# Optimization experiments

Measured on AMD Instinct MI355X. Metric: run time of the kernel, lower is better.

Reference implementation:

```python
import jax, jax.numpy as jnp
import numpy as np

B, N, D_MEM, D_HID = 64, 65536, 1024, 1024


def setup_inputs() -> dict:
    key = jax.random.key(0)
    k1, k2, k3 = jax.random.split(key, 3)
    memory_bank = jax.random.normal(k1, (N, D_MEM), dtype=jnp.float32)
    decoder_state = jax.random.normal(k2, (B, D_HID), dtype=jnp.float32)
    # nn.Linear(memory_bank_size -> hidden_size, bias=False): weight [D_HID, D_MEM]
    W = jax.random.normal(k3, (D_HID, D_MEM), dtype=jnp.float32) / np.sqrt(D_MEM)
    # ragged tree sizes summing exactly to N (concrete, built on host)
    rng = np.random.default_rng(0)
    lens = rng.integers(512, 1536, size=B).astype(np.float64)
    lens = np.maximum(1, np.floor(lens * N / lens.sum()).astype(np.int64))
    lens[-1] += N - lens.sum()
    return {
        "memory_bank": memory_bank,
        "decoder_state": decoder_state,
        "W": W,
        "tree_node_num_lst": jnp.asarray(lens, dtype=jnp.int64),
    }


def reference(memory_bank, decoder_state, W, tree_node_num_lst):
    # segment id per node: tree index it belongs to (total_repeat_length keeps it jit-able)
    n_total = memory_bank.shape[0]
    batch = decoder_state.shape[0]
    seg = jnp.repeat(jnp.arange(batch), tree_node_num_lst, total_repeat_length=n_total)  # [N]
    # memory_project: one big GEMM instead of per-tree launches
    enc = memory_bank @ W.T                                  # [N, D_HID]
    # per-node score = <decoder_state[tree], enc[node]>
    scores = jnp.sum(enc * decoder_state[seg], axis=-1)      # [N]
    # segment (per-tree) stable softmax
    m = jax.ops.segment_max(scores, seg, num_segments=batch)  # [B]
    e = jnp.exp(scores - m[seg])                              # [N]
    z = jax.ops.segment_sum(e, seg, num_segments=batch)       # [B]
    attn = e / z[seg]                                         # [N]
    # context = attn-weighted sum of raw memory bank per tree
    context = jax.ops.segment_sum(attn[:, None] * memory_bank, seg, num_segments=batch)  # [B, D_MEM]
    return context
```

## Files before the change

### kernel.cpp

```cpp
#include <hip/hip_runtime.h>
#include <math.h>

#define B_TREES 64
#define N_NODES 65536
#define D 1024
#define D4 (D/4)

#define CHUNK 64
#define SUB 8
#define NSUB (CHUNK/SUB)
#define NCHUNK (N_NODES/CHUNK)
#define NSLOT (2*NCHUNK)

__global__ void offsets_kernel(const int* __restrict__ lens32, int* __restrict__ off) {
    if (threadIdx.x == 0 && blockIdx.x == 0) {
        long long s32 = 0;
        for (int b = 0; b < B_TREES; ++b) s32 += lens32[b];
        const bool is32 = (s32 == (long long)N_NODES);
        int acc = 0;
        off[0] = 0;
        for (int b = 0; b < B_TREES; ++b) {
            int len = is32 ? lens32[b] : (int)(((const long long*)lens32)[b]);
            acc += len;
            off[b + 1] = acc;
        }
    }
}

__global__ void v_kernel(const float* __restrict__ ds, const float* __restrict__ W,
                         float* __restrict__ v) {
    const int m  = blockIdx.x * 256 + threadIdx.x;
    const int b0 = blockIdx.y * 4;
    const int h0 = blockIdx.z * 128;
    float acc[4] = {0.f, 0.f, 0.f, 0.f};
    for (int h = h0; h < h0 + 128; ++h) {
        float wv = W[h * D + m];
        #pragma unroll
        for (int j = 0; j < 4; ++j)
            acc[j] += ds[(b0 + j) * D + h] * wv;
    }
    #pragma unroll
    for (int j = 0; j < 4; ++j)
        atomicAdd(&v[(b0 + j) * D + m], acc[j]);
}

__global__ __launch_bounds__(256) void fused_kernel(
    const float4* __restrict__ mb, const float4* __restrict__ v,
    const int* __restrict__ off,
    float* __restrict__ m_arr, float* __restrict__ z_arr,
    int* __restrict__ seg_arr, float4* __restrict__ vec)
{
    __shared__ float4 smb[SUB * D4];
    __shared__ float  ssc[SUB];
    __shared__ int    sinfo[2];

    const int tid  = threadIdx.x;
    const int wave = tid >> 6;
    const int lane = tid & 63;
    const int c    = blockIdx.x;
    const int n0   = c * CHUNK;

    if (tid == 0) {
        int lo = 0, hi = B_TREES - 1;
        while (lo < hi) { int mid = (lo + hi + 1) >> 1; if (off[mid] <= n0) lo = mid; else hi = mid - 1; }
        sinfo[0] = lo;
        const int nxt = off[lo + 1];
        sinfo[1] = (nxt < n0 + CHUNK) ? nxt : 0x7fffffff;
    }
    __syncthreads();
    const int sa   = sinfo[0];
    const int cutg = sinfo[1];
    const bool two = (cutg != 0x7fffffff);

    float  m0 = -INFINITY, z0 = 0.f, m1 = -INFINITY, z1 = 0.f;
    float4 a0 = make_float4(0.f, 0.f, 0.f, 0.f);
    float4 a1 = make_float4(0.f, 0.f, 0.f, 0.f);

    float4 vr0, vr1, vr2, vr3;
    int vcur = -1;

    for (int st = 0; st < NSUB; ++st) {
        const int nb = n0 + st * SUB;
        #pragma unroll
        for (int k = 0; k < SUB; ++k)
            smb[k * D4 + tid] = mb[(size_t)(nb + k) * D4 + tid];
        __syncthreads();

        #pragma unroll
        for (int q = 0; q < 2; ++q) {
            const int k  = wave * 2 + q;
            const int sg = (nb + k < cutg) ? sa : sa + 1;
            if (sg != vcur) {
                vcur = sg;
                vr0 = v[(size_t)sg * D4 +   0 + lane];
                vr1 = v[(size_t)sg * D4 +  64 + lane];
                vr2 = v[(size_t)sg * D4 + 128 + lane];
                vr3 = v[(size_t)sg * D4 + 192 + lane];
            }
            const float4 b0v = smb[k * D4 +   0 + lane];
            const float4 b1v = smb[k * D4 +  64 + lane];
            const float4 b2v = smb[k * D4 + 128 + lane];
            const float4 b3v = smb[k * D4 + 192 + lane];
            float acc = b0v.x*vr0.x + b0v.y*vr0.y + b0v.z*vr0.z + b0v.w*vr0.w;
            acc      += b1v.x*vr1.x + b1v.y*vr1.y + b1v.z*vr1.z + b1v.w*vr1.w;
            acc      += b2v.x*vr2.x + b2v.y*vr2.y + b2v.z*vr2.z + b2v.w*vr2.w;
            acc      += b3v.x*vr3.x + b3v.y*vr3.y + b3v.z*vr3.z + b3v.w*vr3.w;
            #pragma unroll
            for (int o = 32; o > 0; o >>= 1) acc += __shfl_down(acc, o, 64);
            if (lane == 0) ssc[k] = acc;
        }
        __syncthreads();

        #pragma unroll
        for (int k = 0; k < SUB; ++k) {
            const float  s    = ssc[k];
            const float4 arow = smb[k * D4 + tid];
            if (nb + k < cutg) {
                if (s > m0) {
                    const float sc = __expf(m0 - s);
                    z0 *= sc; a0.x *= sc; a0.y *= sc; a0.z *= sc; a0.w *= sc;
                    m0 = s;
                }
                const float w = __expf(s - m0);
                z0 += w;
                a0.x += w * arow.x; a0.y += w * arow.y; a0.z += w * arow.z; a0.w += w * arow.w;
            } else {
                if (s > m1) {
                    const float sc = __expf(m1 - s);
                    z1 *= sc; a1.x *= sc; a1.y *= sc; a1.z *= sc; a1.w *= sc;
                    m1 = s;
                }
                const float w = __expf(s - m1);
                z1 += w;
                a1.x += w * arow.x; a1.y += w * arow.y; a1.z += w * arow.z; a1.w += w * arow.w;
            }
        }
        __syncthreads();
    }

    const int slot0 = 2 * c, slot1 = 2 * c + 1;
    vec[(size_t)slot0 * D4 + tid] = a0;
    if (tid == 0) { m_arr[slot0] = m0; z_arr[slot0] = z0; seg_arr[slot0] = sa; }
    if (two) {
        vec[(size_t)slot1 * D4 + tid] = a1;
        if (tid == 0) { m_arr[slot1] = m1; z_arr[slot1] = z1; seg_arr[slot1] = sa + 1; }
    } else if (tid == 0) {
        seg_arr[slot1] = -1;
    }
}

__global__ __launch_bounds__(256) void combine_kernel(
    const int* __restrict__ off, const float* __restrict__ m_arr,
    const float* __restrict__ z_arr, const int* __restrict__ seg_arr,
    const float4* __restrict__ vec, float4* __restrict__ out)
{
    const int b = blockIdx.x, t = threadIdx.x;
    const int s0 = off[b], s1 = off[b + 1];
    const int c0 = s0 / CHUNK, c1 = (s1 - 1) / CHUNK;

    float mseg = -INFINITY;
    for (int cc = c0; cc <= c1; ++cc) {
        #pragma unroll
        for (int j = 0; j < 2; ++j) {
            const int sl = 2 * cc + j;
            if (seg_arr[sl] == b) mseg = fmaxf(mseg, m_arr[sl]);
        }
    }
    float zseg = 0.f;
    float4 acc = make_float4(0.f, 0.f, 0.f, 0.f);
    for (int cc = c0; cc <= c1; ++cc) {
        #pragma unroll
        for (int j = 0; j < 2; ++j) {
            const int sl = 2 * cc + j;
            if (seg_arr[sl] == b) {
                const float sc = __expf(m_arr[sl] - mseg);
                zseg += sc * z_arr[sl];
                const float4 vv = vec[(size_t)sl * D4 + t];
                acc.x += sc * vv.x; acc.y += sc * vv.y;
                acc.z += sc * vv.z; acc.w += sc * vv.w;
            }
        }
    }
    const float inv = 1.f / zseg;
    acc.x *= inv; acc.y *= inv; acc.z *= inv; acc.w *= inv;
    out[(size_t)b * D4 + t] = acc;
}

extern "C" void kernel_launch(void* const* d_in, const int* in_sizes, int n_in,
                              void* d_out, int out_size, void* d_ws, size_t ws_size,
                              hipStream_t stream) {
    const float* mb   = (const float*)d_in[0];
    const float* ds   = (const float*)d_in[1];
    const float* W    = (const float*)d_in[2];
    const int*   lens = (const int*)d_in[3];
    float*       out  = (float*)d_out;

    char*  ws      = (char*)d_ws;
    int*   off     = (int*)ws;
    float* v       = (float*)(ws + 512);
    float* m_arr   = (float*)(ws + 512 + 64 * D * 4);
    float* z_arr   = m_arr + NSLOT;
    int*   seg_arr = (int*)(z_arr + NSLOT);
    float* vec     = (float*)((char*)(seg_arr + NSLOT));

    hipMemsetAsync(v, 0, 64 * D * sizeof(float), stream);

    offsets_kernel<<<1, 64, 0, stream>>>(lens, off);

    {
        dim3 grid(4, 16, 8);
        v_kernel<<<grid, 256, 0, stream>>>(ds, W, v);
    }

    fused_kernel<<<NCHUNK, 256, 0, stream>>>(
        (const float4*)mb, (const float4*)v, off, m_arr, z_arr, seg_arr, (float4*)vec);

    combine_kernel<<<B_TREES, 256, 0, stream>>>(
        off, m_arr, z_arr, seg_arr, (const float4*)vec, (float4*)out);
}
```

Measured before the change: 406.3 us.

## Prefetch memory bank rows into registers, drop memset and offsets kernel

```diff
diff --git a/kernel.cpp b/kernel.cpp
--- a/kernel.cpp
+++ b/kernel.cpp
@@ -11,27 +11,36 @@
 #define NSUB (CHUNK/SUB)
 #define NCHUNK (N_NODES/CHUNK)
 #define NSLOT (2*NCHUNK)
-
-__global__ void offsets_kernel(const int* __restrict__ lens32, int* __restrict__ off) {
-    if (threadIdx.x == 0 && blockIdx.x == 0) {
-        long long s32 = 0;
-        for (int b = 0; b < B_TREES; ++b) s32 += lens32[b];
-        const bool is32 = (s32 == (long long)N_NODES);
-        int acc = 0;
-        off[0] = 0;
-        for (int b = 0; b < B_TREES; ++b) {
-            int len = is32 ? lens32[b] : (int)(((const long long*)lens32)[b]);
-            acc += len;
-            off[b + 1] = acc;
-        }
-    }
-}
-
-__global__ void v_kernel(const float* __restrict__ ds, const float* __restrict__ W,
-                         float* __restrict__ v) {
+#define VZ 8
+
+__device__ __forceinline__ void block_offsets(const int* __restrict__ lens32,
+                                              int* __restrict__ soff,
+                                              int tid, int lane) {
+    if ((tid >> 6) == 0) {
+        long long x32 = (long long)lens32[lane];
+        long long tot = x32;
+        #pragma unroll
+        for (int o = 32; o > 0; o >>= 1) tot += __shfl_xor(tot, o, 64);
+        int len = (tot == (long long)N_NODES) ? (int)x32
+                                              : (int)(((const long long*)lens32)[lane]);
+        int scan = len;
+        #pragma unroll
+        for (int o = 1; o < 64; o <<= 1) {
+            int y = __shfl_up(scan, o, 64);
+            if (lane >= o) scan += y;
+        }
+        soff[lane + 1] = scan;
+        if (lane == 0) soff[0] = 0;
+    }
+}
+
+__global__ __launch_bounds__(256) void v_kernel(const float* __restrict__ ds,
+                                                const float* __restrict__ W,
+                                                float* __restrict__ v_part) {
     const int m  = blockIdx.x * 256 + threadIdx.x;
     const int b0 = blockIdx.y * 4;
-    const int h0 = blockIdx.z * 128;
+    const int z  = blockIdx.z;
+    const int h0 = z * 128;
     float acc[4] = {0.f, 0.f, 0.f, 0.f};
     for (int h = h0; h < h0 + 128; ++h) {
         float wv = W[h * D + m];
@@ -41,18 +50,18 @@
     }
     #pragma unroll
     for (int j = 0; j < 4; ++j)
-        atomicAdd(&v[(b0 + j) * D + m], acc[j]);
-}
-
-__global__ __launch_bounds__(256) void fused_kernel(
-    const float4* __restrict__ mb, const float4* __restrict__ v,
-    const int* __restrict__ off,
+        v_part[((size_t)(z * B_TREES + b0 + j)) * D + m] = acc[j];
+}
+
+__global__ __launch_bounds__(256, 4) void fused_kernel(
+    const float4* __restrict__ mb, const float4* __restrict__ v_part,
+    const int* __restrict__ lens32,
     float* __restrict__ m_arr, float* __restrict__ z_arr,
     int* __restrict__ seg_arr, float4* __restrict__ vec)
 {
     __shared__ float4 smb[SUB * D4];
     __shared__ float  ssc[SUB];
-    __shared__ int    sinfo[2];
+    __shared__ int    soff[B_TREES + 1];
 
     const int tid  = threadIdx.x;
     const int wave = tid >> 6;
@@ -60,16 +69,19 @@
     const int c    = blockIdx.x;
     const int n0   = c * CHUNK;
 
-    if (tid == 0) {
-        int lo = 0, hi = B_TREES - 1;
-        while (lo < hi) { int mid = (lo + hi + 1) >> 1; if (off[mid] <= n0) lo = mid; else hi = mid - 1; }
-        sinfo[0] = lo;
-        const int nxt = off[lo + 1];
-        sinfo[1] = (nxt < n0 + CHUNK) ? nxt : 0x7fffffff;
-    }
+    float4 pf[SUB];
+    #pragma unroll
+    for (int k = 0; k < SUB; ++k)
+        pf[k] = mb[(size_t)(n0 + k) * D4 + tid];
+
+    block_offsets(lens32, soff, tid, lane);
     __syncthreads();
-    const int sa   = sinfo[0];
-    const int cutg = sinfo[1];
+
+    int lo = 0, hi = B_TREES - 1;
+    while (lo < hi) { int mid = (lo + hi + 1) >> 1; if (soff[mid] <= n0) lo = mid; else hi = mid - 1; }
+    const int sa   = lo;
+    const int nxt  = soff[sa + 1];
+    const int cutg = (nxt < n0 + CHUNK) ? nxt : 0x7fffffff;
     const bool two = (cutg != 0x7fffffff);
 
     float  m0 = -INFINITY, z0 = 0.f, m1 = -INFINITY, z1 = 0.f;
@@ -81,10 +93,18 @@
 
     for (int st = 0; st < NSUB; ++st) {
         const int nb = n0 + st * SUB;
+
         #pragma unroll
         for (int k = 0; k < SUB; ++k)
-            smb[k * D4 + tid] = mb[(size_t)(nb + k) * D4 + tid];
+            smb[k * D4 + tid] = pf[k];
         __syncthreads();
+
+        if (st + 1 < NSUB) {
+            const int nb2 = nb + SUB;
+            #pragma unroll
+            for (int k = 0; k < SUB; ++k)
+                pf[k] = mb[(size_t)(nb2 + k) * D4 + tid];
+        }
 
         #pragma unroll
         for (int q = 0; q < 2; ++q) {
@@ -92,10 +112,16 @@
             const int sg = (nb + k < cutg) ? sa : sa + 1;
             if (sg != vcur) {
                 vcur = sg;
-                vr0 = v[(size_t)sg * D4 +   0 + lane];
-                vr1 = v[(size_t)sg * D4 +  64 + lane];
-                vr2 = v[(size_t)sg * D4 + 128 + lane];
-                vr3 = v[(size_t)sg * D4 + 192 + lane];
+                vr0 = make_float4(0.f,0.f,0.f,0.f); vr1 = vr0; vr2 = vr0; vr3 = vr0;
+                #pragma unroll
+                for (int z = 0; z < VZ; ++z) {
+                    const float4* vp = v_part + (size_t)(z * B_TREES + sg) * D4;
+                    float4 t;
+                    t = vp[  0 + lane]; vr0.x+=t.x; vr0.y+=t.y; vr0.z+=t.z; vr0.w+=t.w;
+                    t = vp[ 64 + lane]; vr1.x+=t.x; vr1.y+=t.y; vr1.z+=t.z; vr1.w+=t.w;
+                    t = vp[128 + lane]; vr2.x+=t.x; vr2.y+=t.y; vr2.z+=t.z; vr2.w+=t.w;
+                    t = vp[192 + lane]; vr3.x+=t.x; vr3.y+=t.y; vr3.z+=t.z; vr3.w+=t.w;
+                }
             }
             const float4 b0v = smb[k * D4 +   0 + lane];
             const float4 b1v = smb[k * D4 +  64 + lane];
@@ -150,12 +176,17 @@
 }
 
 __global__ __launch_bounds__(256) void combine_kernel(
-    const int* __restrict__ off, const float* __restrict__ m_arr,
+    const int* __restrict__ lens32, const float* __restrict__ m_arr,
     const float* __restrict__ z_arr, const int* __restrict__ seg_arr,
     const float4* __restrict__ vec, float4* __restrict__ out)
 {
-    const int b = blockIdx.x, t = threadIdx.x;
-    const int s0 = off[b], s1 = off[b + 1];
+    __shared__ int soff[B_TREES + 1];
+    const int t = threadIdx.x, lane = t & 63;
+    block_offsets(lens32, soff, t, lane);
+    __syncthreads();
+
+    const int b  = blockIdx.x;
+    const int s0 = soff[b], s1 = soff[b + 1];
     const int c0 = s0 / CHUNK, c1 = (s1 - 1) / CHUNK;
 
     float mseg = -INFINITY;
@@ -196,25 +227,21 @@
     float*       out  = (float*)d_out;
 
     char*  ws      = (char*)d_ws;
-    int*   off     = (int*)ws;
-    float* v       = (float*)(ws + 512);
-    float* m_arr   = (float*)(ws + 512 + 64 * D * 4);
+    float* v_part  = (float*)ws;
+    float* m_arr   = (float*)(ws + (size_t)VZ * B_TREES * D * 4);
     float* z_arr   = m_arr + NSLOT;
     int*   seg_arr = (int*)(z_arr + NSLOT);
     float* vec     = (float*)((char*)(seg_arr + NSLOT));
 
-    hipMemsetAsync(v, 0, 64 * D * sizeof(float), stream);
-
-    offsets_kernel<<<1, 64, 0, stream>>>(lens, off);
-
     {
-        dim3 grid(4, 16, 8);
-        v_kernel<<<grid, 256, 0, stream>>>(ds, W, v);
+        dim3 grid(4, 16, VZ);
+        v_kernel<<<grid, 256, 0, stream>>>(ds, W, v_part);
     }
 
     fused_kernel<<<NCHUNK, 256, 0, stream>>>(
-        (const float4*)mb, (const float4*)v, off, m_arr, z_arr, seg_arr, (float4*)vec);
+        (const float4*)mb, (const float4*)v_part, lens,
+        m_arr, z_arr, seg_arr, (float4*)vec);
 
     combine_kernel<<<B_TREES, 256, 0, stream>>>(
-        off, m_arr, z_arr, seg_arr, (const float4*)vec, (float4*)out);
-}
+        lens, m_arr, z_arr, seg_arr, (const float4*)vec, (float4*)out);
+}
```

Result: slower. 431.2 us (+6.1%).
